# Optimization experiments

Measured on AMD Instinct MI355X. Metric: run time of the kernel, lower is better.

Reference implementation:

```python
import jax, jax.numpy as jnp
import numpy as np

N = 100000       # nodes
E = 1600000      # edges (before self loops)
F_IN = 128       # input features
H = 4            # heads
C1, C2 = 32, 16  # per-head channels of conv1/conv2


def setup_inputs() -> dict:
    key = jax.random.key(0)
    ks = jax.random.split(key, 12)
    x = jax.random.normal(ks[0], (N, F_IN), jnp.float32)
    edge_index = jax.random.randint(ks[1], (2, E), 0, N, dtype=jnp.int32)
    s1 = 1.0 / np.sqrt(F_IN)
    s2 = 1.0 / np.sqrt(H * C1)
    return {
        "x": x,
        "edge_index": edge_index,
        "W1": jax.random.normal(ks[2], (F_IN, H * C1), jnp.float32) * s1,
        "a_src1": jax.random.normal(ks[3], (1, H, C1), jnp.float32) * s1,
        "a_dst1": jax.random.normal(ks[4], (1, H, C1), jnp.float32) * s1,
        "b1": jnp.zeros((H * C1,), jnp.float32),
        "W2": jax.random.normal(ks[5], (H * C1, H * C2), jnp.float32) * s2,
        "a_src2": jax.random.normal(ks[6], (1, H, C2), jnp.float32) * s2,
        "a_dst2": jax.random.normal(ks[7], (1, H, C2), jnp.float32) * s2,
        "b2": jnp.zeros((H * C2,), jnp.float32),
        "fc_w": jax.random.normal(ks[8], (H * C2, 2), jnp.float32) * (1.0 / np.sqrt(H * C2)),
        "fc_b": jnp.zeros((2,), jnp.float32),
    }


def gat_layer(x, edge_index, W, a_src, a_dst, b, heads, ch):
    """PyG GATConv: concat=True, negative_slope=0.2 (self loops already in edge_index)."""
    n = x.shape[0]
    h = (x @ W).reshape(n, heads, ch)                      # [N,H,C]
    alpha_src = jnp.sum(h * a_src, axis=-1)                # [N,H]
    alpha_dst = jnp.sum(h * a_dst, axis=-1)                # [N,H]
    src, dst = edge_index[0], edge_index[1]                # edge j->i: src=j, dst=i
    e = jax.nn.leaky_relu(alpha_src[src] + alpha_dst[dst], 0.2)  # [E,H]
    # scatter-softmax over incoming edges of each destination node
    m = jax.ops.segment_max(e, dst, num_segments=n)
    m = jnp.where(jnp.isfinite(m), m, 0.0)
    ex = jnp.exp(e - m[dst])
    s = jax.ops.segment_sum(ex, dst, num_segments=n)
    alpha = ex / s[dst]                                    # self loops guarantee s > 0
    out = jax.ops.segment_sum(alpha[:, :, None] * h[src], dst, num_segments=n)
    return out.reshape(n, heads * ch) + b


def reference(x, edge_index, W1, a_src1, a_dst1, b1, W2, a_src2, a_dst2, b2, fc_w, fc_b):
    n = x.shape[0]
    loops = jnp.arange(n, dtype=edge_index.dtype)
    ei = jnp.concatenate([edge_index, jnp.stack([loops, loops])], axis=1)  # add self loops once
    h = jax.nn.relu(gat_layer(x, ei, W1, a_src1, a_dst1, b1, H, C1))
    h = gat_layer(h, ei, W2, a_src2, a_dst2, b2, H, C2)
    g = jnp.sum(h, axis=0, keepdims=True)  # global_add_pool, batch = all zeros -> single graph
    return g @ fc_w + fc_b
```

## Files before the change

kernel.cpp:

```cpp
#include <hip/hip_runtime.h>
#include <hip/hip_bf16.h>
#include <math.h>


using pkh2 = decltype(__builtin_amdgcn_cvt_pkrtz(0.f, 0.f));
typedef __fp16 half8v __attribute__((ext_vector_type(8)));
typedef __attribute__((ext_vector_type(4))) float f32x4;

__device__ __forceinline__ unsigned cvt2h(float a, float b) {
    pkh2 r = __builtin_amdgcn_cvt_pkrtz(a, b);
    return __builtin_bit_cast(unsigned, r);
}
__device__ __forceinline__ unsigned short f2h(float f) {
    return __builtin_bit_cast(unsigned short, (_Float16)f);
}

__device__ __forceinline__ float fdot2b(unsigned wp, unsigned hp, float c) {
#if __has_builtin(__builtin_amdgcn_fdot2)
    return __builtin_amdgcn_fdot2(__builtin_bit_cast(pkh2, wp),
                                  __builtin_bit_cast(pkh2, hp), c, false);
#else
    pkh2 w = __builtin_bit_cast(pkh2, wp), h = __builtin_bit_cast(pkh2, hp);
    return fmaf((float)w[0], (float)h[0], fmaf((float)w[1], (float)h[1], c));
#endif
}


__global__ void init_k(int* __restrict__ bucketCnt, float* __restrict__ g) {
    int i = threadIdx.x;
    if (i < 512) bucketCnt[i] = 0;
    if (i < 66)  g[i] = 0.f;
}

__global__ void bucket_hist_k(const int* __restrict__ ei, int* __restrict__ bucketCnt,
                              int E, int N, int NB) {
    __shared__ int cnt[512];
    for (int t = threadIdx.x; t < 512; t += blockDim.x) cnt[t] = 0;
    __syncthreads();
    const int ITEMS = E + N;
    for (int i = blockIdx.x * blockDim.x + threadIdx.x; i < ITEMS;
         i += gridDim.x * blockDim.x) {
        int d = (i < E) ? ei[E + i] : (i - E);
        atomicAdd(&cnt[d >> 8], 1);
    }
    __syncthreads();
    for (int t = threadIdx.x; t < NB; t += blockDim.x)
        if (cnt[t]) atomicAdd(&bucketCnt[t], cnt[t]);
}

__global__ void bucket_scan_k(const int* __restrict__ bucketCnt,
                              int* __restrict__ bucketOff,
                              int* __restrict__ bucketFill, int NB) {
    __shared__ int ls[512];
    int t = threadIdx.x;
    int v = (t < NB) ? bucketCnt[t] : 0;
    ls[t] = v;
    __syncthreads();
    for (int off = 1; off < 512; off <<= 1) {
        int a = (t >= off) ? ls[t - off] : 0;
        __syncthreads();
        ls[t] += a;
        __syncthreads();
    }
    if (t < NB) { int e = ls[t] - v; bucketOff[t] = e; bucketFill[t] = e; }
}

__global__ __launch_bounds__(256) void bin_scatter_k(const int* __restrict__ ei,
                                                     int* __restrict__ bucketFill,
                                                     int2* __restrict__ binned,
                                                     int E, int N) {
    __shared__ int cnt[512];
    __shared__ int base[512];
    const int ITEMS = E + N;
    const int t = threadIdx.x;
    const int chunk0 = blockIdx.x * 4096;
    for (int b = t; b < 512; b += 256) cnt[b] = 0;
    __syncthreads();
    int s[16], d[16], r[16];
#pragma unroll
    for (int j = 0; j < 16; j++) {
        int i = chunk0 + j * 256 + t;
        if (i < ITEMS) {
            if (i < E) { s[j] = ei[i]; d[j] = ei[E + i]; }
            else       { s[j] = d[j] = i - E; }
            r[j] = atomicAdd(&cnt[d[j] >> 8], 1);
        } else d[j] = -1;
    }
    __syncthreads();
    for (int b = t; b < 512; b += 256) {
        int c = cnt[b];
        base[b] = c ? atomicAdd(&bucketFill[b], c) : 0;
    }
    __syncthreads();
#pragma unroll
    for (int j = 0; j < 16; j++)
        if (d[j] >= 0) binned[base[d[j] >> 8] + r[j]] = make_int2(s[j], d[j]);
}

__global__ void node_offs_k(const int2* __restrict__ binned,
                            const int* __restrict__ bucketOff,
                            const int* __restrict__ bucketCnt,
                            int* __restrict__ offs, int N, int ITEMS) {
    __shared__ int cnt[256];
    __shared__ int ls[256];
    const int b = blockIdx.x;
    const int t = threadIdx.x;
    cnt[t] = 0;
    __syncthreads();
    const int beg = bucketOff[b], c = bucketCnt[b];
    for (int i = t; i < c; i += 256)
        atomicAdd(&cnt[binned[beg + i].y & 255], 1);
    __syncthreads();
    int v = cnt[t];
    ls[t] = v;
    __syncthreads();
    for (int off = 1; off < 256; off <<= 1) {
        int a = (t >= off) ? ls[t - off] : 0;
        __syncthreads();
        ls[t] += a;
        __syncthreads();
    }
    int node = b * 256 + t;
    if (node < N) offs[node] = beg + ls[t] - v;
    if (node == N - 1) offs[N] = ITEMS;
}

__global__ void csr_scatter_k(const int2* __restrict__ binned,
                              const int* __restrict__ bucketOff,
                              const int* __restrict__ bucketCnt,
                              const int* __restrict__ offs, int* __restrict__ csr) {
    __shared__ int fill[256];
    const int b = blockIdx.x;
    fill[threadIdx.x] = 0;
    __syncthreads();
    const int beg = bucketOff[b], c = bucketCnt[b];
    for (int i = threadIdx.x; i < c; i += 256) {
        int2 sd = binned[beg + i];
        int r = atomicAdd(&fill[sd.y & 255], 1);
        csr[offs[sd.y] + r] = sd.x;
    }
}


template<int NCOL, bool XF16>
__global__ __launch_bounds__(256) void gemm_alpha_mfma(
        const void* __restrict__ Xv, const float* __restrict__ W,
        const float* __restrict__ asrc, const float* __restrict__ adst,
        unsigned short* __restrict__ Y, float* __restrict__ As,
        float* __restrict__ Ad, int M) {
    constexpr int NT = NCOL / 16;
    __shared__ alignas(16) short alds[4 * 4 * 64 * 8];
    __shared__ alignas(16) short blds[NT * 4 * 64 * 8];

    const int t    = threadIdx.x;
    const int w    = t >> 6, lane = t & 63;
    const int row0 = blockIdx.x * 64;

    if constexpr (!XF16) {
        const float* X = (const float*)Xv;
#pragma unroll
        for (int i = 0; i < 8; i++) {
            int flat = (i * 256 + t) * 4;
            int r = flat >> 7, k0 = flat & 127;
            int gr = row0 + r;
            float4 v = make_float4(0.f, 0.f, 0.f, 0.f);
            if (gr < M) v = *(const float4*)&X[(size_t)gr * 128 + k0];
            uint2 u = make_uint2(cvt2h(v.x, v.y), cvt2h(v.z, v.w));
            int frag = ((r >> 4) * 4 + (k0 >> 5)) * 64 + ((((k0 & 31) >> 3) << 4) | (r & 15));
            *(uint2*)&alds[frag * 8 + (k0 & 7)] = u;
        }
    } else {
        const unsigned short* X = (const unsigned short*)Xv;
#pragma unroll
        for (int i = 0; i < 4; i++) {
            int flat = (i * 256 + t) * 8;
            int r = flat >> 7, k0 = flat & 127;
            int gr = row0 + r;
            uint4 v = make_uint4(0u, 0u, 0u, 0u);
            if (gr < M) v = *(const uint4*)&X[(size_t)gr * 128 + k0];
            int frag = ((r >> 4) * 4 + (k0 >> 5)) * 64 + ((((k0 & 31) >> 3) << 4) | (r & 15));
            *(uint4*)&alds[frag * 8] = v;
        }
    }

    {
        constexpr int KQ = 256 / NCOL;
        constexpr int BITER = 32 / KQ;
        int c = t % NCOL, kq = t / NCOL;
        int nt = c >> 4, n = c & 15;
#pragma unroll
        for (int i = 0; i < BITER; i++) {
            int k0 = (i * KQ + kq) * 4;
            uint2 u = make_uint2(
                cvt2h(W[(size_t)(k0 + 0) * NCOL + c], W[(size_t)(k0 + 1) * NCOL + c]),
                cvt2h(W[(size_t)(k0 + 2) * NCOL + c], W[(size_t)(k0 + 3) * NCOL + c]));
            int frag = (nt * 4 + (k0 >> 5)) * 64 + ((((k0 & 31) >> 3) << 4) | n);
            *(uint2*)&blds[frag * 8 + (k0 & 7)] = u;
        }
    }
    __syncthreads();

    f32x4 acc[NT];
#pragma unroll
    for (int nt = 0; nt < NT; nt++) acc[nt] = (f32x4){0.f, 0.f, 0.f, 0.f};
#pragma unroll
    for (int ks = 0; ks < 4; ks++) {
        half8v a = *(half8v*)&alds[((w * 4 + ks) * 64 + lane) * 8];
#pragma unroll
        for (int nt = 0; nt < NT; nt++) {
            half8v b = *(half8v*)&blds[((nt * 4 + ks) * 64 + lane) * 8];
            acc[nt] = __builtin_amdgcn_mfma_f32_16x16x32_f16(a, b, acc[nt], 0, 0, 0);
        }
    }

    const int g = lane >> 4, col = lane & 15;
    float ps[4][4] = {}, pd[4][4] = {};
#pragma unroll
    for (int nt = 0; nt < NT; nt++) {
        float av = asrc[nt * 16 + col];
        float dv = adst[nt * 16 + col];
        int h = (NCOL == 128) ? (nt >> 1) : nt;
#pragma unroll
        for (int j = 0; j < 4; j++) {
            float v = acc[nt][j];
            ps[j][h] = fmaf(v, av, ps[j][h]);
            pd[j][h] = fmaf(v, dv, pd[j][h]);
            int gr = row0 + w * 16 + 4 * g + j;
            if (gr < M) Y[(size_t)gr * NCOL + nt * 16 + col] = f2h(v);
        }
    }
#pragma unroll
    for (int m = 1; m < 16; m <<= 1) {
#pragma unroll
        for (int j = 0; j < 4; j++)
#pragma unroll
            for (int h = 0; h < 4; h++) {
                ps[j][h] += __shfl_xor(ps[j][h], m);
                pd[j][h] += __shfl_xor(pd[j][h], m);
            }
    }
    if (col == 0) {
#pragma unroll
        for (int j = 0; j < 4; j++) {
            int gr = row0 + w * 16 + 4 * g + j;
            if (gr < M) {
#pragma unroll
                for (int h = 0; h < 4; h++) {
                    As[gr * 4 + h] = ps[j][h];
                    Ad[gr * 4 + h] = pd[j][h];
                }
            }
        }
    }
}


template<bool RELU>
__global__ void agg128_k(const unsigned short* __restrict__ Hb,
                         const float* __restrict__ As, const float* __restrict__ Ad,
                         const int* __restrict__ offs, const int* __restrict__ csr,
                         const float* __restrict__ bias,
                         unsigned short* __restrict__ Outb, int n) {
    int wid  = (blockIdx.x * blockDim.x + threadIdx.x) >> 6;
    int lane = threadIdx.x & 63;
    if (wid >= n) return;
    const int g = lane >> 4;
    const int q = lane & 15;
    const int head = q >> 2;
    const int beg = offs[wid], end = offs[wid + 1];
    const float ad = Ad[wid * 4 + head];
    float acc[8];
#pragma unroll
    for (int k = 0; k < 8; k++) acc[k] = 0.f;
    float sw = 0.f;

    for (int cb = beg; cb < end; cb += 64) {
        const int nc = min(64, end - cb);
        const int sreg = csr[cb + (lane < nc ? lane : 0)];
        const int ncr = (nc + 7) & ~7;
        for (int j = 0; j < ncr; j += 8) {
            const int e0 = j + g, e1 = j + g + 4;
            const bool v0 = e0 < nc, v1 = e1 < nc;
            const int s0 = __shfl(sreg, v0 ? e0 : 0);
            const int s1 = __shfl(sreg, v1 ? e1 : 0);
            const uint4 h0 = *(const uint4*)&Hb[(size_t)s0 * 128 + q * 8];
            const uint4 h1 = *(const uint4*)&Hb[(size_t)s1 * 128 + q * 8];
            float ev0 = As[s0 * 4 + head] + ad; ev0 = ev0 > 0.f ? ev0 : 0.2f * ev0;
            float ev1 = As[s1 * 4 + head] + ad; ev1 = ev1 > 0.f ? ev1 : 0.2f * ev1;
            const float w0 = v0 ? __expf(ev0) : 0.f;
            const float w1 = v1 ? __expf(ev1) : 0.f;
            sw += w0 + w1;
            const unsigned wp = cvt2h(w0, w1);
#pragma unroll
            for (int k = 0; k < 4; k++) {
                unsigned d0 = (&h0.x)[k], d1 = (&h1.x)[k];
                acc[2 * k]     = fdot2b(wp, __builtin_amdgcn_perm(d1, d0, 0x05040100u), acc[2 * k]);
                acc[2 * k + 1] = fdot2b(wp, __builtin_amdgcn_perm(d1, d0, 0x07060302u), acc[2 * k + 1]);
            }
        }
    }

    sw += __shfl_xor(sw, 16); sw += __shfl_xor(sw, 32);
#pragma unroll
    for (int k = 0; k < 8; k++) {
        acc[k] += __shfl_xor(acc[k], 16);
        acc[k] += __shfl_xor(acc[k], 32);
    }
    if (g == 0) {
        const float inv = 1.f / sw;
        float o[8];
#pragma unroll
        for (int k = 0; k < 8; k++) {
            float v = fmaf(acc[k], inv, bias[q * 8 + k]);
            if (RELU) v = fmaxf(v, 0.f);
            o[k] = v;
        }
        uint4 ov = make_uint4(cvt2h(o[0], o[1]), cvt2h(o[2], o[3]),
                              cvt2h(o[4], o[5]), cvt2h(o[6], o[7]));
        *(uint4*)&Outb[(size_t)wid * 128 + q * 8] = ov;
    }
}

__global__ void agg64_k(const unsigned short* __restrict__ Hb,
                        const float* __restrict__ As, const float* __restrict__ Ad,
                        const int* __restrict__ offs, const int* __restrict__ csr,
                        const float* __restrict__ bias,
                        float* __restrict__ Out, int n) {
    int wid  = (blockIdx.x * blockDim.x + threadIdx.x) >> 6;
    int lane = threadIdx.x & 63;
    if (wid >= n) return;
    const int g = lane >> 3;
    const int q = lane & 7;
    const int head = q >> 1;
    const int beg = offs[wid], end = offs[wid + 1];
    const float ad = Ad[wid * 4 + head];
    float acc[8];
#pragma unroll
    for (int k = 0; k < 8; k++) acc[k] = 0.f;
    float sw = 0.f;

    for (int cb = beg; cb < end; cb += 64) {
        const int nc = min(64, end - cb);
        const int sreg = csr[cb + (lane < nc ? lane : 0)];
        const int ncr = (nc + 15) & ~15;
        for (int j = 0; j < ncr; j += 16) {
            const int e0 = j + g, e1 = j + g + 8;
            const bool v0 = e0 < nc, v1 = e1 < nc;
            const int s0 = __shfl(sreg, v0 ? e0 : 0);
            const int s1 = __shfl(sreg, v1 ? e1 : 0);
            const uint4 h0 = *(const uint4*)&Hb[(size_t)s0 * 64 + q * 8];
            const uint4 h1 = *(const uint4*)&Hb[(size_t)s1 * 64 + q * 8];
            float ev0 = As[s0 * 4 + head] + ad; ev0 = ev0 > 0.f ? ev0 : 0.2f * ev0;
            float ev1 = As[s1 * 4 + head] + ad; ev1 = ev1 > 0.f ? ev1 : 0.2f * ev1;
            const float w0 = v0 ? __expf(ev0) : 0.f;
            const float w1 = v1 ? __expf(ev1) : 0.f;
            sw += w0 + w1;
            const unsigned wp = cvt2h(w0, w1);
#pragma unroll
            for (int k = 0; k < 4; k++) {
                unsigned d0 = (&h0.x)[k], d1 = (&h1.x)[k];
                acc[2 * k]     = fdot2b(wp, __builtin_amdgcn_perm(d1, d0, 0x05040100u), acc[2 * k]);
                acc[2 * k + 1] = fdot2b(wp, __builtin_amdgcn_perm(d1, d0, 0x07060302u), acc[2 * k + 1]);
            }
        }
    }

    sw += __shfl_xor(sw, 8); sw += __shfl_xor(sw, 16); sw += __shfl_xor(sw, 32);
#pragma unroll
    for (int k = 0; k < 8; k++) {
        acc[k] += __shfl_xor(acc[k], 8);
        acc[k] += __shfl_xor(acc[k], 16);
        acc[k] += __shfl_xor(acc[k], 32);
    }
    if (g == 0) {
        const float inv = 1.f / sw;
        float4 o0, o1;
        o0.x = fmaf(acc[0], inv, bias[q * 8 + 0]);
        o0.y = fmaf(acc[1], inv, bias[q * 8 + 1]);
        o0.z = fmaf(acc[2], inv, bias[q * 8 + 2]);
        o0.w = fmaf(acc[3], inv, bias[q * 8 + 3]);
        o1.x = fmaf(acc[4], inv, bias[q * 8 + 4]);
        o1.y = fmaf(acc[5], inv, bias[q * 8 + 5]);
        o1.z = fmaf(acc[6], inv, bias[q * 8 + 6]);
        o1.w = fmaf(acc[7], inv, bias[q * 8 + 7]);
        *(float4*)&Out[(size_t)wid * 64 + q * 8]     = o0;
        *(float4*)&Out[(size_t)wid * 64 + q * 8 + 4] = o1;
    }
}


__global__ void pool_k(const float* __restrict__ h2, float* __restrict__ g, int n) {
    __shared__ float ls[256];
    int c   = threadIdx.x & 63;
    int rg  = (blockIdx.x * blockDim.x + threadIdx.x) >> 6;
    int nrg = (gridDim.x * blockDim.x) >> 6;
    float acc = 0.f;
    for (int r = rg; r < n; r += nrg) acc += h2[(size_t)r * 64 + c];
    ls[threadIdx.x] = acc;
    __syncthreads();
    if (threadIdx.x < 64) {
        float v = ls[threadIdx.x] + ls[threadIdx.x + 64] +
                  ls[threadIdx.x + 128] + ls[threadIdx.x + 192];
        atomicAdd(&g[c], v);
    }
}

__global__ void fc_k(const float* __restrict__ g, const float* __restrict__ w,
                     const float* __restrict__ b, float* __restrict__ out) {
    int j = threadIdx.x;
    if (j < 2) {
        float acc = b[j];
        for (int c = 0; c < 64; c++) acc = fmaf(g[c], w[c * 2 + j], acc);
        out[j] = acc;
    }
}


static inline size_t align256(size_t x) { return (x + 255) & ~(size_t)255; }

extern "C" void kernel_launch(void* const* d_in, const int* in_sizes, int n_in,
                              void* d_out, int out_size, void* d_ws, size_t ws_size,
                              hipStream_t stream) {
    const float* x     = (const float*)d_in[0];
    const int*   ei    = (const int*)  d_in[1];
    const float* W1    = (const float*)d_in[2];
    const float* asrc1 = (const float*)d_in[3];
    const float* adst1 = (const float*)d_in[4];
    const float* b1    = (const float*)d_in[5];
    const float* W2    = (const float*)d_in[6];
    const float* asrc2 = (const float*)d_in[7];
    const float* adst2 = (const float*)d_in[8];
    const float* b2    = (const float*)d_in[9];
    const float* fcw   = (const float*)d_in[10];
    const float* fcb   = (const float*)d_in[11];
    float* out = (float*)d_out;

    const int N = in_sizes[0] / 128;
    const int E = in_sizes[1] / 2;
    const int ITEMS = E + N;
    const int NB = (N + 255) >> 8;

    char* w = (char*)d_ws;
    size_t off = 0;
    int* offs  = (int*)(w + off); off = align256(off + (size_t)(N + 1) * 4);
    int* bCnt  = (int*)(w + off); off = align256(off + 512 * 4);
    int* bOff  = (int*)(w + off); off = align256(off + 512 * 4);
    int* bFill = (int*)(w + off); off = align256(off + 512 * 4);
    int* csr   = (int*)(w + off); off = align256(off + (size_t)ITEMS * 4);
    int2* binned = (int2*)(w + off); off = align256(off + (size_t)ITEMS * 8);
    float* As = (float*)(w + off); off = align256(off + (size_t)N * 4 * 4);
    float* Ad = (float*)(w + off); off = align256(off + (size_t)N * 4 * 4);
    float* g  = (float*)(w + off); off = align256(off + 66 * 4);
    unsigned short* bufH = (unsigned short*)(w + off); off = align256(off + (size_t)N * 128 * 2);
    unsigned short* bufO = (unsigned short*)(w + off); off = align256(off + (size_t)N * 128 * 4);
    float* out2 = (float*)bufO;

    init_k<<<1, 512, 0, stream>>>(bCnt, g);
    bucket_hist_k<<<1024, 256, 0, stream>>>(ei, bCnt, E, N, NB);
    bucket_scan_k<<<1, 512, 0, stream>>>(bCnt, bOff, bFill, NB);
    bin_scatter_k<<<(ITEMS + 4095) / 4096, 256, 0, stream>>>(ei, bFill, binned, E, N);
    node_offs_k<<<NB, 256, 0, stream>>>(binned, bOff, bCnt, offs, N, ITEMS);
    csr_scatter_k<<<NB, 256, 0, stream>>>(binned, bOff, bCnt, offs, csr);

    gemm_alpha_mfma<128, false><<<(N + 63) / 64, 256, 0, stream>>>(
        x, W1, asrc1, adst1, bufH, As, Ad, N);
    agg128_k<true><<<(N * 64 + 255) / 256, 256, 0, stream>>>(
        bufH, As, Ad, offs, csr, b1, bufO, N);

    gemm_alpha_mfma<64, true><<<(N + 63) / 64, 256, 0, stream>>>(
        bufO, W2, asrc2, adst2, bufH, As, Ad, N);
    agg64_k<<<(N * 64 + 255) / 256, 256, 0, stream>>>(
        bufH, As, Ad, offs, csr, b2, out2, N);

    pool_k<<<256, 256, 0, stream>>>(out2, g, N);
    fc_k<<<1, 64, 0, stream>>>(g, fcw, fcb, out);
}
```

Before: 272.6 us.

## Fuse layer-2 aggregation with global pooling and unroll gather loops by four

The second-layer aggregation kernel now reduces each node's output straight into a shared-memory pooled vector and then atomically into the global sum, so the separate pool kernel and the N×64 float output write and re-read go away. The bias term is folded into the final FC as n*b2. Both aggregation kernels also process four neighbours per iteration instead of two, which gives more independent gathers in flight. Costs are shared-memory atomics per node, more registers per thread, and a float summation order that differs from before.

```diff
diff --git a/kernel.cpp b/kernel.cpp
--- a/kernel.cpp
+++ b/kernel.cpp
@@ -277,25 +277,37 @@
     for (int cb = beg; cb < end; cb += 64) {
         const int nc = min(64, end - cb);
         const int sreg = csr[cb + (lane < nc ? lane : 0)];
-        const int ncr = (nc + 7) & ~7;
-        for (int j = 0; j < ncr; j += 8) {
-            const int e0 = j + g, e1 = j + g + 4;
-            const bool v0 = e0 < nc, v1 = e1 < nc;
+        const int ncr = (nc + 15) & ~15;
+        for (int j = 0; j < ncr; j += 16) {
+            const int e0 = j + g, e1 = e0 + 4, e2 = e0 + 8, e3 = e0 + 12;
+            const bool v0 = e0 < nc, v1 = e1 < nc, v2 = e2 < nc, v3 = e3 < nc;
             const int s0 = __shfl(sreg, v0 ? e0 : 0);
             const int s1 = __shfl(sreg, v1 ? e1 : 0);
-            const uint4 h0 = *(const uint4*)&Hb[(size_t)s0 * 128 + q * 8];
-            const uint4 h1 = *(const uint4*)&Hb[(size_t)s1 * 128 + q * 8];
+            const int s2 = __shfl(sreg, v2 ? e2 : 0);
+            const int s3 = __shfl(sreg, v3 ? e3 : 0);
+            const uint4 hA = *(const uint4*)&Hb[(size_t)s0 * 128 + q * 8];
+            const uint4 hB = *(const uint4*)&Hb[(size_t)s1 * 128 + q * 8];
+            const uint4 hC = *(const uint4*)&Hb[(size_t)s2 * 128 + q * 8];
+            const uint4 hD = *(const uint4*)&Hb[(size_t)s3 * 128 + q * 8];
             float ev0 = As[s0 * 4 + head] + ad; ev0 = ev0 > 0.f ? ev0 : 0.2f * ev0;
             float ev1 = As[s1 * 4 + head] + ad; ev1 = ev1 > 0.f ? ev1 : 0.2f * ev1;
+            float ev2 = As[s2 * 4 + head] + ad; ev2 = ev2 > 0.f ? ev2 : 0.2f * ev2;
+            float ev3 = As[s3 * 4 + head] + ad; ev3 = ev3 > 0.f ? ev3 : 0.2f * ev3;
             const float w0 = v0 ? __expf(ev0) : 0.f;
             const float w1 = v1 ? __expf(ev1) : 0.f;
-            sw += w0 + w1;
-            const unsigned wp = cvt2h(w0, w1);
+            const float w2 = v2 ? __expf(ev2) : 0.f;
+            const float w3 = v3 ? __expf(ev3) : 0.f;
+            sw += (w0 + w1) + (w2 + w3);
+            const unsigned wp01 = cvt2h(w0, w1);
+            const unsigned wp23 = cvt2h(w2, w3);
 #pragma unroll
             for (int k = 0; k < 4; k++) {
-                unsigned d0 = (&h0.x)[k], d1 = (&h1.x)[k];
-                acc[2 * k]     = fdot2b(wp, __builtin_amdgcn_perm(d1, d0, 0x05040100u), acc[2 * k]);
-                acc[2 * k + 1] = fdot2b(wp, __builtin_amdgcn_perm(d1, d0, 0x07060302u), acc[2 * k + 1]);
+                unsigned a0 = (&hA.x)[k], a1 = (&hB.x)[k];
+                unsigned a2 = (&hC.x)[k], a3 = (&hD.x)[k];
+                acc[2 * k]     = fdot2b(wp01, __builtin_amdgcn_perm(a1, a0, 0x05040100u), acc[2 * k]);
+                acc[2 * k]     = fdot2b(wp23, __builtin_amdgcn_perm(a3, a2, 0x05040100u), acc[2 * k]);
+                acc[2 * k + 1] = fdot2b(wp01, __builtin_amdgcn_perm(a1, a0, 0x07060302u), acc[2 * k + 1]);
+                acc[2 * k + 1] = fdot2b(wp23, __builtin_amdgcn_perm(a3, a2, 0x07060302u), acc[2 * k + 1]);
             }
         }
     }
@@ -321,96 +333,92 @@
     }
 }
 
-__global__ void agg64_k(const unsigned short* __restrict__ Hb,
-                        const float* __restrict__ As, const float* __restrict__ Ad,
-                        const int* __restrict__ offs, const int* __restrict__ csr,
-                        const float* __restrict__ bias,
-                        float* __restrict__ Out, int n) {
-    int wid  = (blockIdx.x * blockDim.x + threadIdx.x) >> 6;
-    int lane = threadIdx.x & 63;
-    if (wid >= n) return;
+
+__global__ void agg64_pool_k(const unsigned short* __restrict__ Hb,
+                             const float* __restrict__ As, const float* __restrict__ Ad,
+                             const int* __restrict__ offs, const int* __restrict__ csr,
+                             float* __restrict__ gOut, int n) {
+    __shared__ float gl[64];
+    const int t = threadIdx.x;
+    if (t < 64) gl[t] = 0.f;
+    __syncthreads();
+    const int wid  = (blockIdx.x * blockDim.x + t) >> 6;
+    const int lane = t & 63;
     const int g = lane >> 3;
     const int q = lane & 7;
     const int head = q >> 1;
-    const int beg = offs[wid], end = offs[wid + 1];
-    const float ad = Ad[wid * 4 + head];
+    const bool active = wid < n;
     float acc[8];
 #pragma unroll
     for (int k = 0; k < 8; k++) acc[k] = 0.f;
     float sw = 0.f;
 
-    for (int cb = beg; cb < end; cb += 64) {
-        const int nc = min(64, end - cb);
-        const int sreg = csr[cb + (lane < nc ? lane : 0)];
-        const int ncr = (nc + 15) & ~15;
-        for (int j = 0; j < ncr; j += 16) {
-            const int e0 = j + g, e1 = j + g + 8;
-            const bool v0 = e0 < nc, v1 = e1 < nc;
-            const int s0 = __shfl(sreg, v0 ? e0 : 0);
-            const int s1 = __shfl(sreg, v1 ? e1 : 0);
-            const uint4 h0 = *(const uint4*)&Hb[(size_t)s0 * 64 + q * 8];
-            const uint4 h1 = *(const uint4*)&Hb[(size_t)s1 * 64 + q * 8];
-            float ev0 = As[s0 * 4 + head] + ad; ev0 = ev0 > 0.f ? ev0 : 0.2f * ev0;
-            float ev1 = As[s1 * 4 + head] + ad; ev1 = ev1 > 0.f ? ev1 : 0.2f * ev1;
-            const float w0 = v0 ? __expf(ev0) : 0.f;
-            const float w1 = v1 ? __expf(ev1) : 0.f;
-            sw += w0 + w1;
-            const unsigned wp = cvt2h(w0, w1);
-#pragma unroll
-            for (int k = 0; k < 4; k++) {
-                unsigned d0 = (&h0.x)[k], d1 = (&h1.x)[k];
-                acc[2 * k]     = fdot2b(wp, __builtin_amdgcn_perm(d1, d0, 0x05040100u), acc[2 * k]);
-                acc[2 * k + 1] = fdot2b(wp, __builtin_amdgcn_perm(d1, d0, 0x07060302u), acc[2 * k + 1]);
+    if (active) {
+        const int beg = offs[wid], end = offs[wid + 1];
+        const float ad = Ad[wid * 4 + head];
+        for (int cb = beg; cb < end; cb += 64) {
+            const int nc = min(64, end - cb);
+            const int sreg = csr[cb + (lane < nc ? lane : 0)];
+            const int ncr = (nc + 31) & ~31;
+            for (int j = 0; j < ncr; j += 32) {
+                const int e0 = j + g, e1 = e0 + 8, e2 = e0 + 16, e3 = e0 + 24;
+                const bool v0 = e0 < nc, v1 = e1 < nc, v2 = e2 < nc, v3 = e3 < nc;
+                const int s0 = __shfl(sreg, v0 ? e0 : 0);
+                const int s1 = __shfl(sreg, v1 ? e1 : 0);
+                const int s2 = __shfl(sreg, v2 ? e2 : 0);
+                const int s3 = __shfl(sreg, v3 ? e3 : 0);
+                const uint4 hA = *(const uint4*)&Hb[(size_t)s0 * 64 + q * 8];
+                const uint4 hB = *(const uint4*)&Hb[(size_t)s1 * 64 + q * 8];
+                const uint4 hC = *(const uint4*)&Hb[(size_t)s2 * 64 + q * 8];
+                const uint4 hD = *(const uint4*)&Hb[(size_t)s3 * 64 + q * 8];
+                float ev0 = As[s0 * 4 + head] + ad; ev0 = ev0 > 0.f ? ev0 : 0.2f * ev0;
+                float ev1 = As[s1 * 4 + head] + ad; ev1 = ev1 > 0.f ? ev1 : 0.2f * ev1;
+                float ev2 = As[s2 * 4 + head] + ad; ev2 = ev2 > 0.f ? ev2 : 0.2f * ev2;
+                float ev3 = As[s3 * 4 + head] + ad; ev3 = ev3 > 0.f ? ev3 : 0.2f * ev3;
+                const float w0 = v0 ? __expf(ev0) : 0.f;
+                const float w1 = v1 ? __expf(ev1) : 0.f;
+                const float w2 = v2 ? __expf(ev2) : 0.f;
+                const float w3 = v3 ? __expf(ev3) : 0.f;
+                sw += (w0 + w1) + (w2 + w3);
+                const unsigned wp01 = cvt2h(w0, w1);
+                const unsigned wp23 = cvt2h(w2, w3);
+#pragma unroll
+                for (int k = 0; k < 4; k++) {
+                    unsigned a0 = (&hA.x)[k], a1 = (&hB.x)[k];
+                    unsigned a2 = (&hC.x)[k], a3 = (&hD.x)[k];
+                    acc[2 * k]     = fdot2b(wp01, __builtin_amdgcn_perm(a1, a0, 0x05040100u), acc[2 * k]);
+                    acc[2 * k]     = fdot2b(wp23, __builtin_amdgcn_perm(a3, a2, 0x05040100u), acc[2 * k]);
+                    acc[2 * k + 1] = fdot2b(wp01, __builtin_amdgcn_perm(a1, a0, 0x07060302u), acc[2 * k + 1]);
+                    acc[2 * k + 1] = fdot2b(wp23, __builtin_amdgcn_perm(a3, a2, 0x07060302u), acc[2 * k + 1]);
+                }
             }
         }
-    }
-
-    sw += __shfl_xor(sw, 8); sw += __shfl_xor(sw, 16); sw += __shfl_xor(sw, 32);
-#pragma unroll
-    for (int k = 0; k < 8; k++) {
-        acc[k] += __shfl_xor(acc[k], 8);
-        acc[k] += __shfl_xor(acc[k], 16);
-        acc[k] += __shfl_xor(acc[k], 32);
-    }
-    if (g == 0) {
-        const float inv = 1.f / sw;
-        float4 o0, o1;
-        o0.x = fmaf(acc[0], inv, bias[q * 8 + 0]);
-        o0.y = fmaf(acc[1], inv, bias[q * 8 + 1]);
-        o0.z = fmaf(acc[2], inv, bias[q * 8 + 2]);
-        o0.w = fmaf(acc[3], inv, bias[q * 8 + 3]);
-        o1.x = fmaf(acc[4], inv, bias[q * 8 + 4]);
-        o1.y = fmaf(acc[5], inv, bias[q * 8 + 5]);
-        o1.z = fmaf(acc[6], inv, bias[q * 8 + 6]);
-        o1.w = fmaf(acc[7], inv, bias[q * 8 + 7]);
-        *(float4*)&Out[(size_t)wid * 64 + q * 8]     = o0;
-        *(float4*)&Out[(size_t)wid * 64 + q * 8 + 4] = o1;
-    }
-}
-
-
-__global__ void pool_k(const float* __restrict__ h2, float* __restrict__ g, int n) {
-    __shared__ float ls[256];
-    int c   = threadIdx.x & 63;
-    int rg  = (blockIdx.x * blockDim.x + threadIdx.x) >> 6;
-    int nrg = (gridDim.x * blockDim.x) >> 6;
-    float acc = 0.f;
-    for (int r = rg; r < n; r += nrg) acc += h2[(size_t)r * 64 + c];
-    ls[threadIdx.x] = acc;
-    __syncthreads();
-    if (threadIdx.x < 64) {
-        float v = ls[threadIdx.x] + ls[threadIdx.x + 64] +
-                  ls[threadIdx.x + 128] + ls[threadIdx.x + 192];
-        atomicAdd(&g[c], v);
-    }
-}
-
-__global__ void fc_k(const float* __restrict__ g, const float* __restrict__ w,
-                     const float* __restrict__ b, float* __restrict__ out) {
+        sw += __shfl_xor(sw, 8); sw += __shfl_xor(sw, 16); sw += __shfl_xor(sw, 32);
+#pragma unroll
+        for (int k = 0; k < 8; k++) {
+            acc[k] += __shfl_xor(acc[k], 8);
+            acc[k] += __shfl_xor(acc[k], 16);
+            acc[k] += __shfl_xor(acc[k], 32);
+        }
+        if (g == 0) {
+            const float inv = 1.f / sw;
+#pragma unroll
+            for (int k = 0; k < 8; k++) atomicAdd(&gl[q * 8 + k], acc[k] * inv);
+        }
+    }
+    __syncthreads();
+    if (t < 64) atomicAdd(&gOut[t], gl[t]);
+}
+
+
+__global__ void fc_k(const float* __restrict__ g, const float* __restrict__ b2,
+                     const float* __restrict__ w, const float* __restrict__ b,
+                     float* __restrict__ out, int n) {
     int j = threadIdx.x;
     if (j < 2) {
         float acc = b[j];
-        for (int c = 0; c < 64; c++) acc = fmaf(g[c], w[c * 2 + j], acc);
+        for (int c = 0; c < 64; c++)
+            acc = fmaf(g[c] + (float)n * b2[c], w[c * 2 + j], acc);
         out[j] = acc;
     }
 }
@@ -452,8 +460,7 @@
     float* Ad = (float*)(w + off); off = align256(off + (size_t)N * 4 * 4);
     float* g  = (float*)(w + off); off = align256(off + 66 * 4);
     unsigned short* bufH = (unsigned short*)(w + off); off = align256(off + (size_t)N * 128 * 2);
-    unsigned short* bufO = (unsigned short*)(w + off); off = align256(off + (size_t)N * 128 * 4);
-    float* out2 = (float*)bufO;
+    unsigned short* bufO = (unsigned short*)(w + off); off = align256(off + (size_t)N * 128 * 2);
 
     init_k<<<1, 512, 0, stream>>>(bCnt, g);
     bucket_hist_k<<<1024, 256, 0, stream>>>(ei, bCnt, E, N, NB);
@@ -469,9 +476,8 @@
 
     gemm_alpha_mfma<64, true><<<(N + 63) / 64, 256, 0, stream>>>(
         bufO, W2, asrc2, adst2, bufH, As, Ad, N);
-    agg64_k<<<(N * 64 + 255) / 256, 256, 0, stream>>>(
-        bufH, As, Ad, offs, csr, b2, out2, N);
-
-    pool_k<<<256, 256, 0, stream>>>(out2, g, N);
-    fc_k<<<1, 64, 0, stream>>>(g, fcw, fcb, out);
-}
+    agg64_pool_k<<<(N * 64 + 255) / 256, 256, 0, stream>>>(
+        bufH, As, Ad, offs, csr, g, N);
+
+    fc_k<<<1, 64, 0, stream>>>(g, b2, fcw, fcb, out, N);
+}
```

New measurement: 805.0 us. 2.95x slower.
